# Performance work log

Hardware: AMD Instinct MI355X
Metric: run time of the kernel (lower is better)

## Reference

```python
import jax, jax.numpy as jnp
import numpy as np

N_CELLS = 50000


def setup_inputs() -> dict:
    key = jax.random.key(0)
    ks = jax.random.split(key, 8)
    in_dim, emb = 1000, 128
    sl0 = 1.0 / np.sqrt(in_dim)
    sl1 = 1.0 / np.sqrt(emb)
    return {
        "x": jax.random.normal(ks[0], (in_dim, N_CELLS), dtype=jnp.float32),
        "knn_edge_index": jax.random.randint(ks[1], (2, 800000), 0, N_CELLS, dtype=jnp.int64),
        "W_l0": jax.random.normal(ks[2], (emb, in_dim), dtype=jnp.float32) * sl0,
        "b_l0": jnp.zeros((emb,), dtype=jnp.float32),
        "W_r0": jax.random.normal(ks[3], (emb, in_dim), dtype=jnp.float32) * sl0,
        "W_l1": jax.random.normal(ks[4], (emb, emb), dtype=jnp.float32) * sl1,
        "b_l1": jnp.zeros((emb,), dtype=jnp.float32),
        "W_r1": jax.random.normal(ks[5], (emb, emb), dtype=jnp.float32) * sl1,
    }


def _sage_layer(h, src, dst, W_l, b_l, W_r, n_nodes):
    # mean aggregation of source-node features onto target nodes (PyG SAGEConv default)
    agg = jax.ops.segment_sum(h[src], dst, num_segments=n_nodes)      # [N, d_in]
    cnt = jax.ops.segment_sum(jnp.ones((src.shape[0],), h.dtype), dst,
                              num_segments=n_nodes)                   # [N]
    mean_nbr = agg / jnp.maximum(cnt, 1.0)[:, None]
    out = mean_nbr @ W_l.T + b_l + h @ W_r.T                          # [N, d_out]
    return jax.nn.elu(out)  # dropout is identity in eval mode


def reference(x, knn_edge_index, W_l0, b_l0, W_r0, W_l1, b_l1, W_r1):
    src, dst = knn_edge_index[0], knn_edge_index[1]
    h = x.T                                            # (num_cells, num_genes)
    n = h.shape[0]
    h = _sage_layer(h, src, dst, W_l0, b_l0, W_r0, n)
    h = _sage_layer(h, src, dst, W_l1, b_l1, W_r1, n)
    return h
```

## Files before the change

### kernel.cpp

```cpp
#include <hip/hip_runtime.h>
#include <hip/hip_bf16.h>


#define IN_DIM 1000

#define KBARRIER() asm volatile("s_waitcnt lgkmcnt(0)\n\ts_barrier" ::: "memory")

typedef __attribute__((ext_vector_type(8))) short bf16x8;
typedef __attribute__((ext_vector_type(4))) float f32x4;

static __device__ __forceinline__ unsigned int f2bf(float f){
  union { float f; unsigned int u; } v; v.f = f;
  return (v.u + 0x7fffu + ((v.u >> 16) & 1u)) >> 16;
}
static __device__ __forceinline__ float bl(unsigned v){
  union { unsigned u; float f; } t; t.u = v << 16; return t.f;
}
static __device__ __forceinline__ float bh(unsigned v){
  union { unsigned u; float f; } t; t.u = v & 0xFFFF0000u; return t.f;
}
static __device__ __forceinline__ void glds16(const void* g, void* lds){
  __builtin_amdgcn_global_load_lds(
      (const __attribute__((address_space(1))) unsigned int*)g,
      (__attribute__((address_space(3))) unsigned int*)lds, 16, 0, 0);
}

__global__ void prep_k(const float* __restrict__ Wl0, const float* __restrict__ Wr0,
                       const float* __restrict__ Wl1, const float* __restrict__ Wr1,
                       unsigned short* __restrict__ img0,
                       unsigned short* __restrict__ img1, int total0, int total1,
                       int* __restrict__ zptr, int zn){
  int idx = blockIdx.x*256 + threadIdx.x;
  if (idx < total0){
    int j  = idx & 7;
    int l  = (idx >> 3) & 63;
    int ks = (idx >> 9) & 1;
    int n  = (idx >> 10) & 3;
    int w  = (idx >> 12) & 3;
    int s  = idx >> 14;
    int row = w*64 + n*16 + (l & 15);
    int k   = s*64 + ks*32 + (l >> 4)*8 + j;
    float val = 0.f;
    if (k < IN_DIM)
      val = (row < 128) ? Wl0[(size_t)row*IN_DIM + k] : Wr0[(size_t)(row-128)*IN_DIM + k];
    img0[idx] = (unsigned short)f2bf(val);
    return;
  }
  idx -= total0;
  if (idx < total1){
    int s   = idx / (256*72);
    int rem = idx % (256*72);
    int n   = rem / 72;
    int e   = rem % 72;
    float val = 0.f;
    if (e < 64){
      int k = s*64 + e;
      if (k < 128) val = (n < 128) ? Wl1[(size_t)n*128 + k] : Wr1[(size_t)(n-128)*128 + k];
    }
    img1[idx] = (unsigned short)f2bf(val);
    return;
  }
  idx -= total1;
  if (idx < zn) zptr[idx] = 0;
}

__global__ void scan1_k(const int* __restrict__ cnt, int* __restrict__ rowp,
                        float* __restrict__ inv, int* __restrict__ bsum,
                        int* __restrict__ ticket, int N, int nb){
  __shared__ int wt[4];
  __shared__ int lastS;
  int bid = blockIdx.x;
  int i = bid*256 + threadIdx.x;
  int lane = threadIdx.x & 63, wid = threadIdx.x >> 6;
  int v = (i < N) ? cnt[i] : 0;
  int sc = v;
  #pragma unroll
  for (int off = 1; off < 64; off <<= 1){
    int o = __shfl_up(sc, off);
    if (lane >= off) sc += o;
  }
  if (lane == 63) wt[wid] = sc;
  __syncthreads();
  if (threadIdx.x == 0){
    int a = 0;
    #pragma unroll
    for (int j = 0; j < 4; ++j){ int t = wt[j]; wt[j] = a; a += t; }
    bsum[bid] = a;
    if (bid == nb-1 && (N & 255)) rowp[N] = a;
  }
  __syncthreads();
  if (i < N){
    rowp[i] = wt[wid] + sc - v;
    inv[i]  = 1.0f / fmaxf((float)v, 1.0f);
  }
  __threadfence();
  if (threadIdx.x == 0){
    int t = __hip_atomic_fetch_add(ticket, 1, __ATOMIC_ACQ_REL, __HIP_MEMORY_SCOPE_AGENT);
    lastS = (t == (int)gridDim.x - 1);
  }
  __syncthreads();
  if (lastS){
    __threadfence();
    int t2 = threadIdx.x;
    int bv = (t2 < nb) ? __hip_atomic_load(&bsum[t2], __ATOMIC_RELAXED,
                                           __HIP_MEMORY_SCOPE_AGENT) : 0;
    int sc2 = bv;
    #pragma unroll
    for (int off = 1; off < 64; off <<= 1){
      int o = __shfl_up(sc2, off);
      if (lane >= off) sc2 += o;
    }
    __syncthreads();
    if (lane == 63) wt[wid] = sc2;
    __syncthreads();
    if (t2 == 0){
      int a = 0;
      #pragma unroll
      for (int j = 0; j < 4; ++j){ int t = wt[j]; wt[j] = a; a += t; }
      bsum[nb] = a;
      if (!(N & 255)) rowp[N] = 0;
    }
    __syncthreads();
    if (t2 < nb) bsum[t2] = wt[wid] + sc2 - bv;
  }
}

__global__ void fill_col_k(const int* __restrict__ ei, int E,
                           const int* __restrict__ rowp, const int* __restrict__ bsum,
                           int* __restrict__ pos, int* __restrict__ col){
  int e = blockIdx.x*blockDim.x + threadIdx.x;
  if (e < E){
    int src = ei[e];
    int dst = ei[(size_t)E + e];
    int p = atomicAdd(&pos[dst], 1);
    col[rowp[dst] + bsum[dst >> 8] + p] = src;
  }
}

__global__ __launch_bounds__(256, 2) void gemm0_count_k(
    const float* __restrict__ x, const unsigned short* __restrict__ B0img,
    unsigned short* __restrict__ ybl, unsigned short* __restrict__ ybr,
    int N, int Ka, int nsteps, int nblk,
    const int* __restrict__ ei, int E, int* __restrict__ cnt){
  if ((int)blockIdx.x >= nblk){
    int idx = ((int)blockIdx.x - nblk)*256 + threadIdx.x;
    if (idx < E) atomicAdd(&cnt[ei[(size_t)E + idx]], 1);
    return;
  }
  __shared__ char AsB[128*144];
  const int tid = threadIdx.x;
  const int c0  = blockIdx.x * 128;
  const int l   = tid & 63, wid = tid >> 6;
  const int nw  = wid * 64;
  const int lr  = l & 15, lq = l >> 4;
  const int c4  = (tid & 31)*4;
  const int kg  = tid >> 5;
  const int ce  = c0 + c4;
  const int ceff = (ce < N) ? ce : 0;

  f32x4 acc[8][4];
  #pragma unroll
  for (int m=0;m<8;++m)
    #pragma unroll
    for (int n=0;n<4;++n) acc[m][n] = (f32x4){0.f,0.f,0.f,0.f};

  const char* bbase = (const char*)B0img + (size_t)wid*8192 + (size_t)l*16;

  float2 xv0[8], xv1[8];
  bf16x8 bf[8];

  auto loadx = [&](int step){
    #pragma unroll
    for (int kk = 0; kk < 8; ++kk){
      int k = step*64 + kg*8 + kk;
      k = (k < Ka) ? k : (Ka - 1);
      const float* p = &x[(size_t)k*N + ceff];
      xv0[kk] = *(const float2*)p;
      xv1[kk] = *(const float2*)(p + 2);
    }
  };
  auto loadB = [&](int s){
    const char* p = bbase + (size_t)s*32768;
    #pragma unroll
    for (int n = 0; n < 4; ++n)
      #pragma unroll
      for (int ks = 0; ks < 2; ++ks)
        bf[n*2+ks] = *(const bf16x8*)(p + n*2048 + ks*1024);
  };
  auto packx = [&](){
    unsigned w0[4], w1[4], w2[4], w3[4];
    #pragma unroll
    for (int j = 0; j < 4; ++j){
      asm("v_cvt_pk_bf16_f32 %0, %1, %2" : "=v"(w0[j]) : "v"(xv0[2*j].x), "v"(xv0[2*j+1].x));
      asm("v_cvt_pk_bf16_f32 %0, %1, %2" : "=v"(w1[j]) : "v"(xv0[2*j].y), "v"(xv0[2*j+1].y));
      asm("v_cvt_pk_bf16_f32 %0, %1, %2" : "=v"(w2[j]) : "v"(xv1[2*j].x), "v"(xv1[2*j+1].x));
      asm("v_cvt_pk_bf16_f32 %0, %1, %2" : "=v"(w3[j]) : "v"(xv1[2*j].y), "v"(xv1[2*j+1].y));
    }
    *(uint4*)&AsB[(c4+0)*144 + kg*16] = make_uint4(w0[0],w0[1],w0[2],w0[3]);
    *(uint4*)&AsB[(c4+1)*144 + kg*16] = make_uint4(w1[0],w1[1],w1[2],w1[3]);
    *(uint4*)&AsB[(c4+2)*144 + kg*16] = make_uint4(w2[0],w2[1],w2[2],w2[3]);
    *(uint4*)&AsB[(c4+3)*144 + kg*16] = make_uint4(w3[0],w3[1],w3[2],w3[3]);
  };
  auto domfma = [&](){
    #pragma unroll
    for (int ks = 0; ks < 2; ++ks){
      bf16x8 a[8];
      #pragma unroll
      for (int m = 0; m < 8; ++m)
        a[m] = *(const bf16x8*)&AsB[(m*16 + lr)*144 + ks*64 + lq*16];
      #pragma unroll
      for (int n = 0; n < 4; ++n)
        #pragma unroll
        for (int m = 0; m < 8; ++m)
          acc[m][n] = __builtin_amdgcn_mfma_f32_16x16x32_bf16(a[m], bf[n*2+ks], acc[m][n], 0, 0, 0);
    }
  };

  loadx(0);
  for (int s = 0; s < nsteps; ++s){
    if (s) KBARRIER();
    loadB(s);
    packx();
    if (s + 1 < nsteps) loadx(s + 1);
    KBARRIER();
    domfma();
  }

  unsigned short* op = (nw < 128) ? ybl : ybr;
  const int       nc = (nw < 128) ? nw : nw - 128;
  #pragma unroll
  for (int m = 0; m < 8; ++m){
    int rbase = c0 + m*16 + lq*4;
    #pragma unroll
    for (int q = 0; q < 4; ++q){
      int r2 = rbase + q;
      if (r2 < N){
        #pragma unroll
        for (int n = 0; n < 4; ++n)
          op[(size_t)r2*128 + nc + n*16 + lr] = (unsigned short)f2bf(acc[m][n][q]);
      }
    }
  }
}

__global__ __launch_bounds__(256, 3) void gemm1_k(
    const void* __restrict__ Ap, const unsigned short* __restrict__ Bimg,
    unsigned short* __restrict__ ybl, unsigned short* __restrict__ ybr,
    int N, int nsteps){
  __shared__ char AsB[64*128];
  __shared__ char BsB[36864];
  const int tid = threadIdx.x;
  const int c0  = blockIdx.x * 64;
  const int l   = tid & 63, wid = tid >> 6;
  const int nw  = wid * 64;
  const int lr  = l & 15, lq = l >> 4;

  f32x4 acc[4][4];
  #pragma unroll
  for (int m=0;m<4;++m)
    #pragma unroll
    for (int n=0;n<4;++n) acc[m][n] = (f32x4){0.f,0.f,0.f,0.f};

  const char* h1b = (const char*)Ap;

  for (int s = 0; s < nsteps; ++s){
    if (s) __syncthreads();
    {
      const char* bsrc = (const char*)Bimg + (size_t)s*36864;
      #pragma unroll
      for (int i = 0; i < 9; ++i){
        int chunk = i*256 + tid;
        glds16(bsrc + (size_t)chunk*16, &BsB[(i*256 + wid*64)*16]);
      }
    }
    #pragma unroll
    for (int i = 0; i < 2; ++i){
      int chunk = i*256 + tid;
      int row = chunk >> 3, cb = (chunk & 7)*16;
      glds16(h1b + (size_t)(c0 + row)*256 + s*128 + cb,
             &AsB[(i*256 + wid*64)*16]);
    }
    __syncthreads();
    #pragma unroll
    for (int ks = 0; ks < 2; ++ks){
      bf16x8 a[4];
      #pragma unroll
      for (int m = 0; m < 4; ++m){
        int row = m*16 + lr;
        int colb = (ks*64 + lq*16) ^ ((row & 7) << 4);
        a[m] = *(const bf16x8*)&AsB[row*128 + colb];
      }
      #pragma unroll
      for (int n = 0; n < 4; ++n){
        bf16x8 b = *(const bf16x8*)&BsB[(nw + n*16 + lr)*144 + ks*64 + lq*16];
        #pragma unroll
        for (int m = 0; m < 4; ++m)
          acc[m][n] = __builtin_amdgcn_mfma_f32_16x16x32_bf16(a[m], b, acc[m][n], 0, 0, 0);
      }
    }
  }
  unsigned short* op  = (nw < 128) ? ybl : ybr;
  const int       nc  = (nw < 128) ? nw : nw - 128;
  #pragma unroll
  for (int m = 0; m < 4; ++m){
    int rbase = c0 + m*16 + lq*4;
    #pragma unroll
    for (int q = 0; q < 4; ++q){
      int r = rbase + q;
      if (r < N){
        #pragma unroll
        for (int n = 0; n < 4; ++n)
          op[(size_t)r*128 + nc + n*16 + lr] = (unsigned short)f2bf(acc[m][n][q]);
      }
    }
  }
}

template<int LAYER>
__global__ void aggregate_k(const unsigned short* __restrict__ ybl,
    const unsigned short* __restrict__ ybr,
    const int* __restrict__ rowp, const int* __restrict__ bsum,
    const int* __restrict__ col,
    const float* __restrict__ inv, const float* __restrict__ bias,
    void* __restrict__ outp, int N){
  int node = blockIdx.x*4 + (threadIdx.x >> 6);
  int l = threadIdx.x & 63;
  if (node >= N) return;
  int b = rowp[node]   + bsum[node >> 8];
  int e = rowp[node+1] + bsum[(node+1) >> 8];
  int f2 = l*2;
  const unsigned* yl = (const unsigned*)ybl;
  float s0=0.f,s1=0.f,t0=0.f,t1=0.f,u0=0.f,u1=0.f,w0=0.f,w1=0.f;
  for (int kb = b; kb < e; kb += 64){
    int rem = e - kb; if (rem > 64) rem = 64;
    int myc = (l < rem) ? col[kb + l] : 0;
    for (int j = 0; j < rem; j += 16){
      unsigned a[16];
      #pragma unroll
      for (int jj = 0; jj < 16; ++jj){
        int src = __shfl(myc, j + jj);
        unsigned v = yl[(size_t)src*64 + l];
        a[jj] = (j + jj < rem) ? v : 0u;
      }
      #pragma unroll
      for (int h = 0; h < 2; ++h){
        s0 += bl(a[h*8+0]); s1 += bh(a[h*8+0]); t0 += bl(a[h*8+1]); t1 += bh(a[h*8+1]);
        u0 += bl(a[h*8+2]); u1 += bh(a[h*8+2]); w0 += bl(a[h*8+3]); w1 += bh(a[h*8+3]);
        s0 += bl(a[h*8+4]); s1 += bh(a[h*8+4]); t0 += bl(a[h*8+5]); t1 += bh(a[h*8+5]);
        u0 += bl(a[h*8+6]); u1 += bh(a[h*8+6]); w0 += bl(a[h*8+7]); w1 += bh(a[h*8+7]);
      }
    }
  }
  s0 = (s0 + t0) + (u0 + w0);
  s1 = (s1 + t1) + (u1 + w1);
  unsigned vs = *(const unsigned*)&ybr[(size_t)node*128 + f2];
  float iv = inv[node];
  float r0 = s0*iv + bias[f2]   + bl(vs);
  float r1 = s1*iv + bias[f2+1] + bh(vs);
  r0 = (r0 > 0.f) ? r0 : expm1f(r0);
  r1 = (r1 > 0.f) ? r1 : expm1f(r1);
  if (LAYER == 0){
    int sf = f2 >> 6, fo = f2 & 63, g = fo >> 3;
    size_t byte = (size_t)node*256 + (size_t)(sf*128 + ((g ^ (node & 7)) << 4) + (fo & 7)*2);
    *(unsigned*)((char*)outp + byte) = f2bf(r0) | (f2bf(r1) << 16);
  } else {
    *(float2*)((float*)outp + (size_t)node*128 + f2) = make_float2(r0, r1);
  }
}

static inline size_t align_up(size_t v, size_t a){ return (v + a - 1) & ~(a - 1); }

extern "C" void kernel_launch(void* const* d_in, const int* in_sizes, int n_in,
                              void* d_out, int out_size, void* d_ws, size_t ws_size,
                              hipStream_t stream) {
  const float* x   = (const float*)d_in[0];
  const int*   ei  = (const int*)d_in[1];
  const float* Wl0 = (const float*)d_in[2];
  const float* bl0 = (const float*)d_in[3];
  const float* Wr0 = (const float*)d_in[4];
  const float* Wl1 = (const float*)d_in[5];
  const float* bl1 = (const float*)d_in[6];
  const float* Wr1 = (const float*)d_in[7];

  int N = in_sizes[0] / IN_DIM;
  int E = in_sizes[1] / 2;

  const int NS0 = 16;
  const int NS1 = 2;
  int nsb = (N + 255) / 256;

  char* base = (char*)d_ws;
  size_t off = 0;
  unsigned short* ybl = (unsigned short*)(base + off); off = align_up(off + (size_t)N*128*2, 256);
  unsigned short* ybr = (unsigned short*)(base + off); off = align_up(off + (size_t)N*128*2, 256);
  float* inv  = (float*)(base + off); off = align_up(off + (size_t)N*4, 256);
  int*   cnt  = (int*)  (base + off); off = align_up(off + (size_t)N*8 + 256, 256);
  int*   pos  = cnt + N;
  int*   ticket = cnt + 2*N;
  int*   rowp = (int*)  (base + off); off = align_up(off + (size_t)(N+1)*4, 256);
  int*   bsum = (int*)  (base + off); off = align_up(off + (size_t)(nsb+1)*4, 256);
  int*   col  = (int*)  (base + off); off = align_up(off + (size_t)E*4, 256);
  unsigned short* B0img = (unsigned short*)(base + off); off = align_up(off + (size_t)524288*2, 256);
  unsigned short* B1img = (unsigned short*)(base + off); off = align_up(off + (size_t)NS1*18432*2, 256);
  void* h1b = d_out;
  (void)ws_size; (void)n_in; (void)out_size;

  int t0n = 524288, t1n = NS1*18432;
  int zn  = 2*N + 64;
  prep_k<<<(t0n+t1n+zn+255)/256, 256, 0, stream>>>(Wl0, Wr0, Wl1, Wr1,
                                                   B0img, B1img, t0n, t1n,
                                                   cnt, zn);

  int nblk = (N + 127) / 128;
  int cblk = (E + 255) / 256;
  int ablk = (N + 3) / 4;
  int nblk1 = (N + 63) / 64;

  gemm0_count_k<<<nblk + cblk, 256, 0, stream>>>(x, B0img, ybl, ybr, N, IN_DIM,
                                                 NS0, nblk, ei, E, cnt);
  scan1_k<<<nsb, 256, 0, stream>>>(cnt, rowp, inv, bsum, ticket, N, nsb);
  fill_col_k<<<(E+255)/256, 256, 0, stream>>>(ei, E, rowp, bsum, pos, col);
  aggregate_k<0><<<ablk, 256, 0, stream>>>(ybl, ybr, rowp, bsum, col, inv, bl0, h1b, N);

  gemm1_k<<<nblk1, 256, 0, stream>>>(h1b, B1img, ybl, ybr, N, NS1);
  aggregate_k<1><<<ablk, 256, 0, stream>>>(ybl, ybr, rowp, bsum, col, inv, bl1, d_out, N);
}
```

Before: 213.6 us.

## Double-buffer x prefetch two steps ahead in gemm0; widen gemm1 tiles to 128 rows

In the first GEMM, x loads now go into two register sets, and the loop is unrolled by two so each step's global loads are issued two steps ahead. This gives more time to hide the latency of the strided x reads. The second GEMM now processes 128 rows per block instead of 64, which doubles accumulator and LDS A-tile size and lowers the occupancy hint from 3 to 2. More reuse of the B tiles per block is traded against higher register pressure and fewer resident waves.

```diff
diff --git a/kernel.cpp b/kernel.cpp
--- a/kernel.cpp
+++ b/kernel.cpp
@@ -166,17 +166,17 @@
 
   const char* bbase = (const char*)B0img + (size_t)wid*8192 + (size_t)l*16;
 
-  float2 xv0[8], xv1[8];
+  float2 xa0[8], xa1[8], xb0[8], xb1[8];
   bf16x8 bf[8];
 
-  auto loadx = [&](int step){
+  auto loadx = [&](int step, float2* v0, float2* v1){
     #pragma unroll
     for (int kk = 0; kk < 8; ++kk){
       int k = step*64 + kg*8 + kk;
       k = (k < Ka) ? k : (Ka - 1);
       const float* p = &x[(size_t)k*N + ceff];
-      xv0[kk] = *(const float2*)p;
-      xv1[kk] = *(const float2*)(p + 2);
+      v0[kk] = *(const float2*)p;
+      v1[kk] = *(const float2*)(p + 2);
     }
   };
   auto loadB = [&](int s){
@@ -187,14 +187,14 @@
       for (int ks = 0; ks < 2; ++ks)
         bf[n*2+ks] = *(const bf16x8*)(p + n*2048 + ks*1024);
   };
-  auto packx = [&](){
+  auto packx = [&](const float2* v0, const float2* v1){
     unsigned w0[4], w1[4], w2[4], w3[4];
     #pragma unroll
     for (int j = 0; j < 4; ++j){
-      asm("v_cvt_pk_bf16_f32 %0, %1, %2" : "=v"(w0[j]) : "v"(xv0[2*j].x), "v"(xv0[2*j+1].x));
-      asm("v_cvt_pk_bf16_f32 %0, %1, %2" : "=v"(w1[j]) : "v"(xv0[2*j].y), "v"(xv0[2*j+1].y));
-      asm("v_cvt_pk_bf16_f32 %0, %1, %2" : "=v"(w2[j]) : "v"(xv1[2*j].x), "v"(xv1[2*j+1].x));
-      asm("v_cvt_pk_bf16_f32 %0, %1, %2" : "=v"(w3[j]) : "v"(xv1[2*j].y), "v"(xv1[2*j+1].y));
+      asm("v_cvt_pk_bf16_f32 %0, %1, %2" : "=v"(w0[j]) : "v"(v0[2*j].x), "v"(v0[2*j+1].x));
+      asm("v_cvt_pk_bf16_f32 %0, %1, %2" : "=v"(w1[j]) : "v"(v0[2*j].y), "v"(v0[2*j+1].y));
+      asm("v_cvt_pk_bf16_f32 %0, %1, %2" : "=v"(w2[j]) : "v"(v1[2*j].x), "v"(v1[2*j+1].x));
+      asm("v_cvt_pk_bf16_f32 %0, %1, %2" : "=v"(w3[j]) : "v"(v1[2*j].y), "v"(v1[2*j+1].y));
     }
     *(uint4*)&AsB[(c4+0)*144 + kg*16] = make_uint4(w0[0],w0[1],w0[2],w0[3]);
     *(uint4*)&AsB[(c4+1)*144 + kg*16] = make_uint4(w1[0],w1[1],w1[2],w1[3]);
@@ -216,14 +216,24 @@
     }
   };
 
-  loadx(0);
-  for (int s = 0; s < nsteps; ++s){
+  loadx(0, xa0, xa1);
+  loadx(1, xb0, xb1);
+
+  for (int s = 0; s < nsteps; s += 2){
     if (s) KBARRIER();
     loadB(s);
-    packx();
-    if (s + 1 < nsteps) loadx(s + 1);
+    packx(xa0, xa1);
+    if (s + 2 < nsteps) loadx(s + 2, xa0, xa1);
     KBARRIER();
     domfma();
+    if (s + 1 < nsteps){
+      KBARRIER();
+      loadB(s + 1);
+      packx(xb0, xb1);
+      if (s + 3 < nsteps) loadx(s + 3, xb0, xb1);
+      KBARRIER();
+      domfma();
+    }
   }
 
   unsigned short* op = (nw < 128) ? ybl : ybr;
@@ -243,21 +253,21 @@
   }
 }
 
-__global__ __launch_bounds__(256, 3) void gemm1_k(
+__global__ __launch_bounds__(256, 2) void gemm1_k(
     const void* __restrict__ Ap, const unsigned short* __restrict__ Bimg,
     unsigned short* __restrict__ ybl, unsigned short* __restrict__ ybr,
     int N, int nsteps){
-  __shared__ char AsB[64*128];
+  __shared__ char AsB[128*128];
   __shared__ char BsB[36864];
   const int tid = threadIdx.x;
-  const int c0  = blockIdx.x * 64;
+  const int c0  = blockIdx.x * 128;
   const int l   = tid & 63, wid = tid >> 6;
   const int nw  = wid * 64;
   const int lr  = l & 15, lq = l >> 4;
 
-  f32x4 acc[4][4];
+  f32x4 acc[8][4];
   #pragma unroll
-  for (int m=0;m<4;++m)
+  for (int m=0;m<8;++m)
     #pragma unroll
     for (int n=0;n<4;++n) acc[m][n] = (f32x4){0.f,0.f,0.f,0.f};
 
@@ -274,7 +284,7 @@
       }
     }
     #pragma unroll
-    for (int i = 0; i < 2; ++i){
+    for (int i = 0; i < 4; ++i){
       int chunk = i*256 + tid;
       int row = chunk >> 3, cb = (chunk & 7)*16;
       glds16(h1b + (size_t)(c0 + row)*256 + s*128 + cb,
@@ -283,9 +293,9 @@
     __syncthreads();
     #pragma unroll
     for (int ks = 0; ks < 2; ++ks){
-      bf16x8 a[4];
-      #pragma unroll
-      for (int m = 0; m < 4; ++m){
+      bf16x8 a[8];
+      #pragma unroll
+      for (int m = 0; m < 8; ++m){
         int row = m*16 + lr;
         int colb = (ks*64 + lq*16) ^ ((row & 7) << 4);
         a[m] = *(const bf16x8*)&AsB[row*128 + colb];
@@ -294,7 +304,7 @@
       for (int n = 0; n < 4; ++n){
         bf16x8 b = *(const bf16x8*)&BsB[(nw + n*16 + lr)*144 + ks*64 + lq*16];
         #pragma unroll
-        for (int m = 0; m < 4; ++m)
+        for (int m = 0; m < 8; ++m)
           acc[m][n] = __builtin_amdgcn_mfma_f32_16x16x32_bf16(a[m], b, acc[m][n], 0, 0, 0);
       }
     }
@@ -302,7 +312,7 @@
   unsigned short* op  = (nw < 128) ? ybl : ybr;
   const int       nc  = (nw < 128) ? nw : nw - 128;
   #pragma unroll
-  for (int m = 0; m < 4; ++m){
+  for (int m = 0; m < 8; ++m){
     int rbase = c0 + m*16 + lq*4;
     #pragma unroll
     for (int q = 0; q < 4; ++q){
@@ -414,7 +424,6 @@
   int nblk = (N + 127) / 128;
   int cblk = (E + 255) / 256;
   int ablk = (N + 3) / 4;
-  int nblk1 = (N + 63) / 64;
 
   gemm0_count_k<<<nblk + cblk, 256, 0, stream>>>(x, B0img, ybl, ybr, N, IN_DIM,
                                                  NS0, nblk, ei, E, cnt);
@@ -422,6 +431,6 @@
   fill_col_k<<<(E+255)/256, 256, 0, stream>>>(ei, E, rowp, bsum, pos, col);
   aggregate_k<0><<<ablk, 256, 0, stream>>>(ybl, ybr, rowp, bsum, col, inv, bl0, h1b, N);
 
-  gemm1_k<<<nblk1, 256, 0, stream>>>(h1b, B1img, ybl, ybr, N, NS1);
+  gemm1_k<<<nblk, 256, 0, stream>>>(h1b, B1img, ybl, ybr, N, NS1);
   aggregate_k<1><<<ablk, 256, 0, stream>>>(ybl, ybr, rowp, bsum, col, inv, bl1, d_out, N);
 }
```

Result: slower. 219.8 us (+2.9%).
